# Kernel tuning notes

Hardware: AMD Instinct MI355X
Metric: run time of the kernel (lower is better)

The kernel has to match this reference:

```python
import jax, jax.numpy as jnp
import numpy as np

B, LP, LH, D, H = 32, 1024, 1024, 256, 256

def setup_inputs() -> dict:
    key = jax.random.key(0)
    k1, k2, k3 = jax.random.split(key, 3)
    premises = jax.random.normal(k1, (B, LP, D), dtype=jnp.float32)
    hypotheses = jax.random.normal(k2, (B, LH, D), dtype=jnp.float32)
    W_F = jax.random.normal(k3, (D, H), dtype=jnp.float32) * (1.0 / np.sqrt(D))
    return {"premises": premises, "hypotheses": hypotheses, "W_F": W_F}

def reference(premises, hypotheses, W_F):
    # Tanh-projected features: F_p = tanh(P @ W_F), F_h = tanh(H @ W_F)
    F_p = jnp.tanh(jnp.einsum('bpd,dh->bph', premises, W_F))   # [B,LP,H]
    F_h = jnp.tanh(jnp.einsum('bqd,dh->bqh', hypotheses, W_F)) # [B,LH,H]
    # Alignment scores e_ij = F_p . F_h
    eijs = jnp.einsum('bph,bqh->bpq', F_p, F_h)                # [B,LP,LH]
    # betas: for each premise token, softmax over hypothesis tokens, weighted sum of hypotheses
    betas = jnp.einsum('bpq,bqd->bpd', jax.nn.softmax(eijs, axis=-1), hypotheses)  # [B,LP,D]
    # alphas: for each hypothesis token, softmax over premise tokens, weighted sum of premises
    alphas = jnp.einsum('bqp,bpd->bqd',
                        jax.nn.softmax(jnp.swapaxes(eijs, 1, 2), axis=-1),
                        premises)                                                   # [B,LH,D]
    return betas, alphas
```

## Files before the change

### kernel.cpp

```cpp
#include <hip/hip_runtime.h>

typedef _Float16 f16;
typedef __attribute__((ext_vector_type(4))) _Float16 f16x4;
typedef __attribute__((ext_vector_type(8))) _Float16 f16x8;
typedef __attribute__((ext_vector_type(4))) float f32x4;
typedef __attribute__((ext_vector_type(16))) float f32x16;
typedef unsigned int u32;

#define BB 32
#define LL 1024
#define DD 256

#define VMCNT(N) asm volatile("s_waitcnt vmcnt(" #N ")" ::: "memory")
#define LGKMCNT0 asm volatile("s_waitcnt lgkmcnt(0)" ::: "memory")

__device__ __forceinline__ void async_copy16(const f16* g, f16* l) {
  __builtin_amdgcn_global_load_lds(
      (const __attribute__((address_space(1))) u32*)(const void*)g,
      (__attribute__((address_space(3))) u32*)(void*)l, 16, 0, 0);
}

__device__ __forceinline__ u32 pack_pkrtz(float a, float b) {
  auto pk = __builtin_amdgcn_cvt_pkrtz(a, b);
  u32 w;
  __builtin_memcpy(&w, &pk, 4);
  return w;
}


__global__ __launch_bounds__(256) void w_to_frag(const float* __restrict__ W,
                                                 f16* __restrict__ WtF) {
  __shared__ float T32[256][33];
  const int tid = threadIdx.x;
  const int N = blockIdx.x;
  const int nn = tid & 31, kr = tid >> 5;
#pragma unroll
  for (int p = 0; p < 32; ++p) {
    int k = p * 8 + kr;
    T32[k][nn] = W[(size_t)k * 256 + N * 32 + nn];
  }
  __syncthreads();
  const int wv = tid >> 6, lane = tid & 63;
  const int l32 = lane & 31, half = lane >> 5;
#pragma unroll
  for (int i = 0; i < 4; ++i) {
    int s = wv * 4 + i;
    f16x8 ov;
#pragma unroll
    for (int j = 0; j < 8; ++j) ov[j] = (f16)T32[s * 16 + half * 8 + j][l32];
    *(f16x8*)&WtF[(size_t)N * 8192 + s * 512 + lane * 8] = ov;
  }
}

__global__ __launch_bounds__(256, 3) void proj_mfma(
    const float* __restrict__ Pin, const float* __restrict__ Hin,
    const f16* __restrict__ WtF, f16* __restrict__ Fp, f16* __restrict__ Fh,
    f16* __restrict__ Vtp, f16* __restrict__ Vth) {
  __shared__ f16 As[64][264];
  const int tid = threadIdx.x;
  const int wv = tid >> 6, lane = tid & 63;
  const int l32 = lane & 31, half = lane >> 5;
  const int wm = wv >> 1, wn = wv & 1;
  const float* A = blockIdx.z ? Hin : Pin;
  f16* F = blockIdx.z ? Fh : Fp;
  f16* VtO = blockIdx.z ? Vth : Vtp;
  const int m0 = blockIdx.x * 64;
  const int T0 = m0 >> 5;

  {
    const int r = tid >> 4;
    const int c4 = (tid & 15) * 4;
#pragma unroll
    for (int pp = 0; pp < 4; ++pp)
#pragma unroll
      for (int ch = 0; ch < 4; ++ch) {
        float4 v =
            *(const float4*)&A[(size_t)(m0 + r + pp * 16) * 256 + ch * 64 + c4];
        f16x4 h4;
        h4[0] = (f16)v.x; h4[1] = (f16)v.y; h4[2] = (f16)v.z; h4[3] = (f16)v.w;
        *(f16x4*)&As[r + pp * 16][ch * 64 + c4] = h4;
      }
  }
  __syncthreads();

  f16x8 af[16];
#pragma unroll
  for (int ks = 0; ks < 16; ++ks)
    af[ks] = *(const f16x8*)&As[wm * 32 + l32][ks * 16 + half * 8];

  {
#pragma unroll
    for (int i = 0; i < 8; ++i) {
      int idx = wv * 8 + i;
      int Tl = idx >> 4;
      int t = (idx >> 1) & 7;
      int qh = idx & 1;
      int qb = Tl * 32 + qh * 16 + half * 8;
      f16x8 ov;
#pragma unroll
      for (int j = 0; j < 8; ++j) ov[j] = As[qb + j][t * 32 + l32];
      *(f16x8*)&VtO[(size_t)(T0 + Tl) * 8192 + t * 1024 + qh * 512 +
                    half * 256 + l32 * 8] = ov;
    }
  }
  __syncthreads();

#pragma unroll
  for (int nc = 0; nc < 4; ++nc) {
    f32x16 acc = (f32x16)(0.f);
#pragma unroll
    for (int ks = 0; ks < 16; ++ks) {
      f16x8 wf = *(const f16x8*)&WtF[(size_t)nc * 16384 + wn * 8192 +
                                     ks * 512 + lane * 8];
      acc = __builtin_amdgcn_mfma_f32_32x32x16_f16(af[ks], wf, acc, 0, 0, 0);
    }
#pragma unroll
    for (int r = 0; r < 16; ++r) {
      float xv = acc[r];
      float e2 = __expf(2.f * xv);
      float th = 1.f - 2.f / (e2 + 1.f);
      As[wm * 32 + (r & 3) + 8 * (r >> 2) + 4 * half]
        [nc * 64 + wn * 32 + l32] = (f16)th;
    }
  }
  __syncthreads();

#pragma unroll
  for (int i = 0; i < 8; ++i) {
    int idx = wv * 8 + i;
    int Tl = idx >> 4;
    int s = idx & 15;
    f16x8 ov = *(const f16x8*)&As[Tl * 32 + l32][s * 16 + half * 8];
    *(f16x8*)&F[(size_t)(T0 + Tl) * 8192 + s * 512 + half * 256 + l32 * 8] =
        ov;
  }
}

__global__ __launch_bounds__(256, 2) void flash_mfma(
    const f16* __restrict__ Fpm, const f16* __restrict__ Fhm,
    const f16* __restrict__ Vth, const f16* __restrict__ Vtp,
    float* __restrict__ Out) {
  __shared__ f16 Kb[2][8192];
  __shared__ f16 Vb[2][8192];

  const int tid = threadIdx.x;
  const int wv = tid >> 6, lane = tid & 63;
  const int l32 = lane & 31, half = lane >> 5;

  const f16* Fq = Fpm;
  const f16* Fk = Fhm;
  const f16* Vt = Vth;
  float* O = Out;
  if (blockIdx.y) { Fq = Fhm; Fk = Fpm; Vt = Vtp; O = Out + (size_t)BB * LL * DD; }

  const int x = blockIdx.x;
  const int b = ((x & 7) << 2) | (x >> 6);
  const int p0 = ((x >> 3) & 7) * 128 + wv * 32;
  const int p = p0 + l32;

  const f16* Fq_b = Fq + (size_t)b * LL * DD;
  const f16* Fk_b = Fk + (size_t)b * LL * DD;
  const f16* Vt_b = Vt + (size_t)b * LL * DD;

  f16x8 qf[16];
  {
    const f16* qt = Fq_b + (size_t)(p >> 5) * 8192 + half * 256 + (p & 31) * 8;
#pragma unroll
    for (int s = 0; s < 16; ++s) qf[s] = *(const f16x8*)&qt[s * 512];
  }

  float m_run = -1e30f, l_run = 0.f;
  f32x16 o[8];
#pragma unroll
  for (int t = 0; t < 8; ++t) o[t] = (f32x16)(0.f);

  auto stage = [&](int buf, int T) {
    const f16* kt = Fk_b + (size_t)T * 8192;
    const f16* vt = Vt_b + (size_t)T * 8192;
#pragma unroll
    for (int ii = 0; ii < 4; ++ii) {
      int i = wv * 4 + ii;
      async_copy16(kt + i * 512 + lane * 8, &Kb[buf][i * 512]);
    }
#pragma unroll
    for (int ii = 0; ii < 4; ++ii) {
      int i = wv * 4 + ii;
      async_copy16(vt + i * 512 + lane * 8, &Vb[buf][i * 512]);
    }
  };

  auto tile_compute = [&](int cur) {
    f32x16 S0 = (f32x16)(0.f), S1 = (f32x16)(0.f);
    __builtin_amdgcn_s_setprio(1);
#pragma unroll
    for (int s = 0; s < 16; s += 2) {
      f16x8 k0 = *(const f16x8*)&Kb[cur][s * 512 + lane * 8];
      S0 = __builtin_amdgcn_mfma_f32_32x32x16_f16(k0, qf[s], S0, 0, 0, 0);
      f16x8 k1 = *(const f16x8*)&Kb[cur][(s + 1) * 512 + lane * 8];
      S1 = __builtin_amdgcn_mfma_f32_32x32x16_f16(k1, qf[s + 1], S1, 0, 0, 0);
    }
    __builtin_amdgcn_s_setprio(0);
    f32x16 S;
#pragma unroll
    for (int r = 0; r < 16; ++r) S[r] = S0[r] + S1[r];

    float mt = S[0];
#pragma unroll
    for (int r = 1; r < 16; ++r) mt = fmaxf(mt, S[r]);
    mt = fmaxf(mt, __shfl_xor(mt, 32, 64));

    const bool keep = __all((int)(mt - m_run <= 8.0f)) != 0;
    const float mn = keep ? m_run : fmaxf(m_run, mt);
    float pe[16];
    float ts = 0.f;
#pragma unroll
    for (int r = 0; r < 16; ++r) {
      pe[r] = __expf(S[r] - mn);
      ts += pe[r];
    }
    ts += __shfl_xor(ts, 32, 64);
    if (!keep) {
      const float alpha = __expf(m_run - mn);
      l_run *= alpha;
      m_run = mn;
#pragma unroll
      for (int t = 0; t < 8; ++t)
#pragma unroll
        for (int r = 0; r < 16; ++r) o[t][r] *= alpha;
    }
    l_run += ts;

    u32 pw[8];
#pragma unroll
    for (int i = 0; i < 8; ++i) pw[i] = pack_pkrtz(pe[2 * i], pe[2 * i + 1]);
    u32 rc[4];
    {
      u32 s0 = half ? pw[0] : pw[2];
      u32 s1 = half ? pw[1] : pw[3];
      u32 s2 = half ? pw[4] : pw[6];
      u32 s3 = half ? pw[5] : pw[7];
      rc[0] = (u32)__shfl_xor((int)s0, 32, 64);
      rc[1] = (u32)__shfl_xor((int)s1, 32, 64);
      rc[2] = (u32)__shfl_xor((int)s2, 32, 64);
      rc[3] = (u32)__shfl_xor((int)s3, 32, 64);
    }
    f16x8 pf[2];
#pragma unroll
    for (int h = 0; h < 2; ++h) {
      u32 tmp[4];
      tmp[0] = half ? rc[2 * h] : pw[4 * h];
      tmp[1] = half ? rc[2 * h + 1] : pw[4 * h + 1];
      tmp[2] = half ? pw[4 * h + 2] : rc[2 * h];
      tmp[3] = half ? pw[4 * h + 3] : rc[2 * h + 1];
      __builtin_memcpy(&pf[h], tmp, 16);
    }

    __builtin_amdgcn_s_setprio(1);
#pragma unroll
    for (int t = 0; t < 8; ++t) {
      f16x8 v0 = *(const f16x8*)&Vb[cur][t * 1024 + lane * 8];
      o[t] = __builtin_amdgcn_mfma_f32_32x32x16_f16(v0, pf[0], o[t], 0, 0, 0);
      f16x8 v1 = *(const f16x8*)&Vb[cur][t * 1024 + 512 + lane * 8];
      o[t] = __builtin_amdgcn_mfma_f32_32x32x16_f16(v1, pf[1], o[t], 0, 0, 0);
    }
    __builtin_amdgcn_s_setprio(0);
  };

  stage(0, 0);
  int cur = 0;
  for (int it = 0; it < 31; ++it) {
    stage(cur ^ 1, it + 1);
    VMCNT(8);
    __builtin_amdgcn_sched_barrier(0);
    __builtin_amdgcn_s_barrier();
    tile_compute(cur);
    __builtin_amdgcn_s_barrier();
    cur ^= 1;
  }
  VMCNT(0);
  __builtin_amdgcn_sched_barrier(0);
  __builtin_amdgcn_s_barrier();
  tile_compute(cur);
  __syncthreads();

  const float inv = 1.f / l_run;
  float* Tw = (float*)&Kb[0][0] + wv * (32 * 36);
  float* Ob = O + (size_t)b * LL * DD;
#pragma unroll
  for (int t = 0; t < 8; ++t) {
#pragma unroll
    for (int g = 0; g < 4; ++g) {
      int C = 2 * g + half;
      f32x4 v;
      v[0] = o[t][4 * g + 0] * inv;
      v[1] = o[t][4 * g + 1] * inv;
      v[2] = o[t][4 * g + 2] * inv;
      v[3] = o[t][4 * g + 3] * inv;
      *(f32x4*)&Tw[l32 * 36 + C * 4] = v;
    }
    LGKMCNT0;
#pragma unroll
    for (int pass = 0; pass < 4; ++pass) {
      int row = pass * 8 + (lane >> 3);
      int Cr = lane & 7;
      f32x4 v = *(const f32x4*)&Tw[row * 36 + Cr * 4];
      *(f32x4*)&Ob[(size_t)(p0 + row) * DD + t * 32 + Cr * 4] = v;
    }
    LGKMCNT0;
  }
}

extern "C" void kernel_launch(void* const* d_in, const int* in_sizes, int n_in,
                              void* d_out, int out_size, void* d_ws,
                              size_t ws_size, hipStream_t stream) {
  const float* premises = (const float*)d_in[0];
  const float* hypotheses = (const float*)d_in[1];
  const float* W = (const float*)d_in[2];
  float* out = (float*)d_out;

  const size_t MF = (size_t)BB * LL * DD;
  f16* Fp = (f16*)d_ws;
  f16* Fh = Fp + MF;
  f16* Vth = Fh + MF;
  f16* Vtp = Vth + MF;
  f16* WtF = (f16*)((char*)d_out + (size_t)out_size * 4 - 256 * 256 * 2);

  w_to_frag<<<dim3(8), 256, 0, stream>>>(W, WtF);
  proj_mfma<<<dim3(512, 1, 2), 256, 0, stream>>>(premises, hypotheses, WtF, Fp,
                                                 Fh, Vtp, Vth);
  flash_mfma<<<dim3(256, 2), 256, 0, stream>>>(Fp, Fh, Vth, Vtp, out);
}
```

Baseline: 209.4 us.

## Software-pipeline QK of next tile with softmax/PV of current; 512-thread blocks

```diff
diff --git a/kernel.cpp b/kernel.cpp
--- a/kernel.cpp
+++ b/kernel.cpp
@@ -136,12 +136,11 @@
   }
 }
 
-__global__ __launch_bounds__(256, 2) void flash_mfma(
+__global__ __launch_bounds__(512, 2) void flash_mfma(
     const f16* __restrict__ Fpm, const f16* __restrict__ Fhm,
     const f16* __restrict__ Vth, const f16* __restrict__ Vtp,
     float* __restrict__ Out) {
-  __shared__ f16 Kb[2][8192];
-  __shared__ f16 Vb[2][8192];
+  __shared__ f16 SMEM[4][8192];
 
   const int tid = threadIdx.x;
   const int wv = tid >> 6, lane = tid & 63;
@@ -154,8 +153,9 @@
   if (blockIdx.y) { Fq = Fhm; Fk = Fpm; Vt = Vtp; O = Out + (size_t)BB * LL * DD; }
 
   const int x = blockIdx.x;
-  const int b = ((x & 7) << 2) | (x >> 6);
-  const int p0 = ((x >> 3) & 7) * 128 + wv * 32;
+  const int b = ((x >> 5) << 3) | (x & 7);
+  const int pblk = (x >> 3) & 3;
+  const int p0 = pblk * 256 + wv * 32;
   const int p = p0 + l32;
 
   const f16* Fq_b = Fq + (size_t)b * LL * DD;
@@ -174,41 +174,35 @@
 #pragma unroll
   for (int t = 0; t < 8; ++t) o[t] = (f32x16)(0.f);
 
-  auto stage = [&](int buf, int T) {
-    const f16* kt = Fk_b + (size_t)T * 8192;
-    const f16* vt = Vt_b + (size_t)T * 8192;
-#pragma unroll
-    for (int ii = 0; ii < 4; ++ii) {
-      int i = wv * 4 + ii;
-      async_copy16(kt + i * 512 + lane * 8, &Kb[buf][i * 512]);
-    }
-#pragma unroll
-    for (int ii = 0; ii < 4; ++ii) {
-      int i = wv * 4 + ii;
-      async_copy16(vt + i * 512 + lane * 8, &Vb[buf][i * 512]);
-    }
-  };
-
-  auto tile_compute = [&](int cur) {
-    f32x16 S0 = (f32x16)(0.f), S1 = (f32x16)(0.f);
+  auto stage_K = [&](int buf, int T) {
+    const f16* kt = Fk_b + (size_t)T * 8192 + wv * 1024 + lane * 8;
+    async_copy16(kt, &SMEM[buf][wv * 1024]);
+    async_copy16(kt + 512, &SMEM[buf][wv * 1024 + 512]);
+  };
+  auto stage_V = [&](int buf, int T) {
+    const f16* vt = Vt_b + (size_t)T * 8192 + wv * 1024 + lane * 8;
+    async_copy16(vt, &SMEM[2 + buf][wv * 1024]);
+    async_copy16(vt + 512, &SMEM[2 + buf][wv * 1024 + 512]);
+  };
+
+  auto qk16 = [&](int buf) {
+    f32x16 S = (f32x16)(0.f);
     __builtin_amdgcn_s_setprio(1);
 #pragma unroll
-    for (int s = 0; s < 16; s += 2) {
-      f16x8 k0 = *(const f16x8*)&Kb[cur][s * 512 + lane * 8];
-      S0 = __builtin_amdgcn_mfma_f32_32x32x16_f16(k0, qf[s], S0, 0, 0, 0);
-      f16x8 k1 = *(const f16x8*)&Kb[cur][(s + 1) * 512 + lane * 8];
-      S1 = __builtin_amdgcn_mfma_f32_32x32x16_f16(k1, qf[s + 1], S1, 0, 0, 0);
+    for (int s = 0; s < 16; ++s) {
+      f16x8 kf = *(const f16x8*)&SMEM[buf][s * 512 + lane * 8];
+      S = __builtin_amdgcn_mfma_f32_32x32x16_f16(kf, qf[s], S, 0, 0, 0);
     }
     __builtin_amdgcn_s_setprio(0);
-    f32x16 S;
-#pragma unroll
-    for (int r = 0; r < 16; ++r) S[r] = S0[r] + S1[r];
-
+    return S;
+  };
+
+  f16x8 pf[2];
+  auto softmax_pack = [&](const f32x16& S) {
     float mt = S[0];
 #pragma unroll
     for (int r = 1; r < 16; ++r) mt = fmaxf(mt, S[r]);
     mt = fmaxf(mt, __shfl_xor(mt, 32, 64));
-
     const bool keep = __all((int)(mt - m_run <= 8.0f)) != 0;
     const float mn = keep ? m_run : fmaxf(m_run, mt);
     float pe[16];
@@ -244,7 +238,6 @@
       rc[2] = (u32)__shfl_xor((int)s2, 32, 64);
       rc[3] = (u32)__shfl_xor((int)s3, 32, 64);
     }
-    f16x8 pf[2];
 #pragma unroll
     for (int h = 0; h < 2; ++h) {
       u32 tmp[4];
@@ -254,37 +247,52 @@
       tmp[3] = half ? pw[4 * h + 3] : rc[2 * h + 1];
       __builtin_memcpy(&pf[h], tmp, 16);
     }
-
+  };
+
+  auto pv = [&](int buf) {
     __builtin_amdgcn_s_setprio(1);
 #pragma unroll
     for (int t = 0; t < 8; ++t) {
-      f16x8 v0 = *(const f16x8*)&Vb[cur][t * 1024 + lane * 8];
+      f16x8 v0 = *(const f16x8*)&SMEM[2 + buf][t * 1024 + lane * 8];
       o[t] = __builtin_amdgcn_mfma_f32_32x32x16_f16(v0, pf[0], o[t], 0, 0, 0);
-      f16x8 v1 = *(const f16x8*)&Vb[cur][t * 1024 + 512 + lane * 8];
+      f16x8 v1 = *(const f16x8*)&SMEM[2 + buf][t * 1024 + 512 + lane * 8];
       o[t] = __builtin_amdgcn_mfma_f32_32x32x16_f16(v1, pf[1], o[t], 0, 0, 0);
     }
     __builtin_amdgcn_s_setprio(0);
   };
 
-  stage(0, 0);
-  int cur = 0;
+  stage_K(0, 0);
+  stage_V(0, 0);
+  stage_K(1, 1);
+  VMCNT(2);
+  __builtin_amdgcn_sched_barrier(0);
+  __builtin_amdgcn_s_barrier();
+  f32x16 Scur = qk16(0);
+  stage_V(1, 1);
+
   for (int it = 0; it < 31; ++it) {
-    stage(cur ^ 1, it + 1);
-    VMCNT(8);
+    const int cur = it & 1, nxt = cur ^ 1;
+    if (it < 30) {
+      stage_K(cur, it + 2);
+      VMCNT(2);
+    } else {
+      VMCNT(0);
+    }
     __builtin_amdgcn_sched_barrier(0);
     __builtin_amdgcn_s_barrier();
-    tile_compute(cur);
+    f32x16 Snext = qk16(nxt);
+    softmax_pack(Scur);
+    pv(cur);
     __builtin_amdgcn_s_barrier();
-    cur ^= 1;
-  }
-  VMCNT(0);
-  __builtin_amdgcn_sched_barrier(0);
-  __builtin_amdgcn_s_barrier();
-  tile_compute(cur);
+    if (it < 30) stage_V(cur, it + 2);
+    Scur = Snext;
+  }
+  softmax_pack(Scur);
+  pv(1);
   __syncthreads();
 
   const float inv = 1.f / l_run;
-  float* Tw = (float*)&Kb[0][0] + wv * (32 * 36);
+  float* Tw = (float*)&SMEM[0][0] + wv * (32 * 36);
   float* Ob = O + (size_t)b * LL * DD;
 #pragma unroll
   for (int t = 0; t < 8; ++t) {
@@ -328,5 +336,5 @@
   w_to_frag<<<dim3(8), 256, 0, stream>>>(W, WtF);
   proj_mfma<<<dim3(512, 1, 2), 256, 0, stream>>>(premises, hypotheses, WtF, Fp,
                                                  Fh, Vtp, Vth);
-  flash_mfma<<<dim3(256, 2), 256, 0, stream>>>(Fp, Fh, Vth, Vtp, out);
-}
+  flash_mfma<<<dim3(128, 2), 512, 0, stream>>>(Fp, Fh, Vth, Vtp, out);
+}
```

New measurement: 205.4 us. No clear change (-1.9%).
